# Kernel optimization log

Measured on AMD Instinct MI355X. Metric: run time of the kernel, lower is better.

Reference implementation:

```python
import jax, jax.numpy as jnp
import numpy as np

TEMP = 2.0   # NTXent uses a hardcoded temperature of 2, not the ctor's 0.07
EPS = 1e-8   # F.cosine_similarity eps


def setup_inputs() -> dict:
    key = jax.random.key(0)
    k1, _ = jax.random.split(key)
    x = jax.random.normal(k1, (8192, 256), dtype=jnp.float32)
    unused = jnp.zeros((1,), dtype=jnp.int32)
    return {"x": x, "unused": unused}


def _cos_matrix(a, b):
    # pairwise cosine similarity: [N, N]
    na = jnp.linalg.norm(a, axis=-1)
    nb = jnp.linalg.norm(b, axis=-1)
    dots = a @ b.T
    return dots / jnp.maximum(na[:, None] * nb[None, :], EPS)


def reference(x, unused):
    n = x.shape[0] // 2
    p, q = x[:n], x[n:]  # anchor, positive

    s_pp = _cos_matrix(p, p)
    s_pn = _cos_matrix(p, q)
    s_nn = _cos_matrix(q, q)
    s_np = _cos_matrix(q, p)

    # double loop i, j in [i, n): upper triangle including diagonal
    mask = jnp.triu(jnp.ones((n, n), dtype=bool))

    exp_sum = (jnp.exp(s_pp / TEMP) + jnp.exp(s_pn / TEMP)
               + jnp.exp(s_nn / TEMP) + jnp.exp(s_np / TEMP))
    sim_all = jnp.sum(jnp.where(mask, exp_sum, 0.0))

    sim_s = jnp.sum(jnp.exp(jnp.diagonal(s_pn) / TEMP))

    return -jnp.log(sim_s / sim_all)
```

## Files before the change

### kernel.cpp

```cpp
#include <hip/hip_runtime.h>

#define DIM     256
#define NROWS   8192
#define NTILE   64
#define NBLK    ((NTILE * (NTILE + 1)) / 2)
#define CHPLANE ((size_t)NROWS * 16)

using i32x4  = __attribute__((ext_vector_type(4))) int;
using i32x8  = __attribute__((ext_vector_type(8))) int;
using f32x16 = __attribute__((ext_vector_type(16))) float;

struct i32x8_pair { i32x4 lo, hi; };

__device__ __forceinline__ unsigned fp4q(float v) {
  float a = fabsf(v);
  unsigned s = (__builtin_bit_cast(unsigned, v) >> 31) << 3;
  unsigned c = a < 0.25f ? 0u : a < 0.75f ? 1u : a < 1.25f ? 2u : a < 1.75f ? 3u
             : a < 2.50f ? 4u : a < 3.50f ? 5u : a < 5.00f ? 6u : 7u;
  return s | c;
}

__device__ __forceinline__ void tile_rc(int t, int& bi, int& bj) {
  int i = (int)((129.0 - sqrt(129.0 * 129.0 - 8.0 * (double)t)) * 0.5);
  while ((i * (129 - i)) / 2 > t) --i;
  while (((i + 1) * (128 - i)) / 2 <= t) ++i;
  bi = i;
  bj = i + (t - (i * (129 - i)) / 2);
}

__device__ __forceinline__ float exp_half(float x) {
  float t = x * 0.7213475204444817f;
  float r;
  asm("v_exp_f32 %0, %1" : "=v"(r) : "v"(t));
  return r;
}

__global__ __launch_bounds__(256) void normalize_k(const float* __restrict__ x,
                                                   unsigned char* __restrict__ z4) {
  const int row  = blockIdx.x * 4 + (threadIdx.x >> 6);
  const int lane = threadIdx.x & 63;
  float4 v = ((const float4*)(x + (size_t)row * DIM))[lane];
  float ss = v.x * v.x + v.y * v.y + v.z * v.z + v.w * v.w;
#pragma unroll
  for (int off = 32; off > 0; off >>= 1) ss += __shfl_xor(ss, off, 64);
  float rn = rsqrtf(fmaxf(ss, 1e-24f)) * 16.0f;
  unsigned c0 = fp4q(v.x * rn), c1 = fp4q(v.y * rn);
  unsigned c2 = fp4q(v.z * rn), c3 = fp4q(v.w * rn);
  unsigned short pk = (unsigned short)((c0 | (c1 << 4)) | ((c2 | (c3 << 4)) << 8));
  *(unsigned short*)(z4 + (size_t)(lane >> 3) * CHPLANE
                        + (size_t)row * 16 + ((2 * lane) & 14)) = pk;
}

__global__ __launch_bounds__(256, 3) void gram_k(const unsigned char* __restrict__ z4,
                                                 double2* __restrict__ partial) {
  __shared__ float red[8];

  const int tid   = threadIdx.x;
  const int lane  = tid & 63;
  const int w     = tid >> 6;
  const int wr    = w >> 1, wc = w & 1;
  const int l31   = lane & 31;
  const int khalf = lane >> 5;

  int bi, bj; tile_rc(blockIdx.x, bi, bj);

  const unsigned char* baseA = z4 + (size_t)khalf * CHPLANE
                             + ((size_t)bi * 128 + wr * 64 + l31) * 16;
  const unsigned char* baseB = z4 + (size_t)khalf * CHPLANE
                             + ((size_t)bj * 128 + wc * 64 + l31) * 16;

  f32x16 acc_f[2][2] = {};
  const i32x4 zero4 = {0, 0, 0, 0};
#pragma unroll
  for (int kc = 0; kc < 4; ++kc) {
    i32x8 a[2], b[2];
#pragma unroll
    for (int t = 0; t < 2; ++t) {
      i32x8_pair pa = { *(const i32x4*)(baseA + (size_t)(2 * kc) * CHPLANE + t * 32 * 16),
                        zero4 };
      a[t] = __builtin_bit_cast(i32x8, pa);
      i32x8_pair pb = { *(const i32x4*)(baseB + (size_t)(2 * kc) * CHPLANE + t * 32 * 16),
                        zero4 };
      b[t] = __builtin_bit_cast(i32x8, pb);
    }
#pragma unroll
    for (int ti = 0; ti < 2; ++ti)
#pragma unroll
      for (int tj = 0; tj < 2; ++tj)
        acc_f[ti][tj] = __builtin_amdgcn_mfma_scale_f32_32x32x64_f8f6f4(
            a[ti], b[tj], acc_f[ti][tj],
            4, 4,
            0, 0x7B7B7B7B,
            0, 0x7B7B7B7B);
  }

  const bool tdiag = (bi == bj);
  const bool sdiag = (bj == bi + 32);
  float lsum = 0.0f, dsum = 0.0f;
  if (tdiag || sdiag) {
#pragma unroll
    for (int ti = 0; ti < 2; ++ti)
#pragma unroll
      for (int tj = 0; tj < 2; ++tj)
#pragma unroll
        for (int r = 0; r < 16; ++r) {
          float e = exp_half(acc_f[ti][tj][r]);
          lsum += e;
          int row_l = (r & 3) + 8 * (r >> 2) + 4 * khalf;
          if (wr == wc && ti == tj && row_l == l31) dsum += e;
        }
  } else {
#pragma unroll
    for (int ti = 0; ti < 2; ++ti)
#pragma unroll
      for (int tj = 0; tj < 2; ++tj)
#pragma unroll
        for (int r = 0; r < 16; ++r)
          lsum += exp_half(acc_f[ti][tj][r]);
  }
#pragma unroll
  for (int off = 32; off > 0; off >>= 1) lsum += __shfl_xor(lsum, off, 64);
  if (tdiag || sdiag) {
#pragma unroll
    for (int off = 32; off > 0; off >>= 1) dsum += __shfl_xor(dsum, off, 64);
  }
  if (lane == 0) { red[w] = lsum; red[4 + w] = dsum; }
  __syncthreads();

  if (tid == 0) {
    float l  = red[0] + red[1] + red[2] + red[3];
    float dd = red[4] + red[5] + red[6] + red[7];
    double2 v;
    v.x = tdiag ? (double)l + (double)dd : 2.0 * (double)l;
    v.y = sdiag ? (double)dd : 0.0;
    partial[blockIdx.x] = v;
  }
}

__global__ __launch_bounds__(256) void reduce_k(const double2* __restrict__ partial,
                                               float* __restrict__ out) {
  __shared__ double redS[4], redD[4];
  double s = 0.0, ss = 0.0;
  for (int i = threadIdx.x; i < NBLK; i += 256) {
    double2 v = partial[i];
    s += v.x; ss += v.y;
  }
#pragma unroll
  for (int off = 32; off > 0; off >>= 1) {
    s  += __shfl_xor(s,  off, 64);
    ss += __shfl_xor(ss, off, 64);
  }
  const int w = threadIdx.x >> 6;
  if ((threadIdx.x & 63) == 0) { redS[w] = s; redD[w] = ss; }
  __syncthreads();
  if (threadIdx.x == 0) {
    double S  = redS[0] + redS[1] + redS[2] + redS[3];
    double sd = redD[0] + redD[1] + redD[2] + redD[3];
    out[0] = (float)(log(0.5 * S + sd) - log(sd));
  }
}

extern "C" void kernel_launch(void* const* d_in, const int* in_sizes, int n_in,
                              void* d_out, int out_size, void* d_ws, size_t ws_size,
                              hipStream_t stream) {
  const float* x    = (const float*)d_in[0];
  unsigned char* z4 = (unsigned char*)d_ws;
  double2* partial  = (double2*)((char*)d_ws + 8 * CHPLANE);
  float* out        = (float*)d_out;

  normalize_k<<<dim3(NROWS / 4), dim3(256), 0, stream>>>(x, z4);
  gram_k<<<dim3(NBLK), dim3(256), 0, stream>>>(z4, partial);
  reduce_k<<<dim3(1), dim3(256), 0, stream>>>(partial, out);
}
```

Measured before the change: 74.33 us.

## Process two tiles per gram block, per-wave partials, batch rows in normalize

Each gram block now handles two upper-triangle tiles in sequence and writes one partial per wave, which removes the shared-memory reduction and the __syncthreads. Per-wave sums are kept in double across both tiles, and the exp sums are split over four float accumulators. The normalize kernel now handles 8 rows per wave with 256 blocks instead of 2048, and gram occupancy is raised to 4 blocks per CU. This trades fewer launches and less sync for less parallelism per launch and register pressure from the higher occupancy target.

```diff
diff --git a/kernel.cpp b/kernel.cpp
--- a/kernel.cpp
+++ b/kernel.cpp
@@ -4,6 +4,8 @@
 #define NROWS   8192
 #define NTILE   64
 #define NBLK    ((NTILE * (NTILE + 1)) / 2)
+#define GB      1040
+#define NPART   (GB * 4)
 #define CHPLANE ((size_t)NROWS * 16)
 
 using i32x4  = __attribute__((ext_vector_type(4))) int;
@@ -37,24 +39,27 @@
 
 __global__ __launch_bounds__(256) void normalize_k(const float* __restrict__ x,
                                                    unsigned char* __restrict__ z4) {
-  const int row  = blockIdx.x * 4 + (threadIdx.x >> 6);
+  const int w    = threadIdx.x >> 6;
   const int lane = threadIdx.x & 63;
-  float4 v = ((const float4*)(x + (size_t)row * DIM))[lane];
-  float ss = v.x * v.x + v.y * v.y + v.z * v.z + v.w * v.w;
+  const int row0 = blockIdx.x * 32 + w * 8;
 #pragma unroll
-  for (int off = 32; off > 0; off >>= 1) ss += __shfl_xor(ss, off, 64);
-  float rn = rsqrtf(fmaxf(ss, 1e-24f)) * 16.0f;
-  unsigned c0 = fp4q(v.x * rn), c1 = fp4q(v.y * rn);
-  unsigned c2 = fp4q(v.z * rn), c3 = fp4q(v.w * rn);
-  unsigned short pk = (unsigned short)((c0 | (c1 << 4)) | ((c2 | (c3 << 4)) << 8));
-  *(unsigned short*)(z4 + (size_t)(lane >> 3) * CHPLANE
-                        + (size_t)row * 16 + ((2 * lane) & 14)) = pk;
+  for (int r = 0; r < 8; ++r) {
+    const int row = row0 + r;
+    float4 v = ((const float4*)(x + (size_t)row * DIM))[lane];
+    float ss = v.x * v.x + v.y * v.y + v.z * v.z + v.w * v.w;
+#pragma unroll
+    for (int off = 32; off > 0; off >>= 1) ss += __shfl_xor(ss, off, 64);
+    float rn = rsqrtf(fmaxf(ss, 1e-24f)) * 16.0f;
+    unsigned c0 = fp4q(v.x * rn), c1 = fp4q(v.y * rn);
+    unsigned c2 = fp4q(v.z * rn), c3 = fp4q(v.w * rn);
+    unsigned short pk = (unsigned short)((c0 | (c1 << 4)) | ((c2 | (c3 << 4)) << 8));
+    *(unsigned short*)(z4 + (size_t)(lane >> 3) * CHPLANE
+                          + (size_t)row * 16 + ((2 * lane) & 14)) = pk;
+  }
 }
 
-__global__ __launch_bounds__(256, 3) void gram_k(const unsigned char* __restrict__ z4,
+__global__ __launch_bounds__(256, 4) void gram_k(const unsigned char* __restrict__ z4,
                                                  double2* __restrict__ partial) {
-  __shared__ float red[8];
-
   const int tid   = threadIdx.x;
   const int lane  = tid & 63;
   const int w     = tid >> 6;
@@ -62,78 +67,79 @@
   const int l31   = lane & 31;
   const int khalf = lane >> 5;
 
-  int bi, bj; tile_rc(blockIdx.x, bi, bj);
+  double accS = 0.0, accD = 0.0;
+  const i32x4 zero4 = {0, 0, 0, 0};
 
-  const unsigned char* baseA = z4 + (size_t)khalf * CHPLANE
-                             + ((size_t)bi * 128 + wr * 64 + l31) * 16;
-  const unsigned char* baseB = z4 + (size_t)khalf * CHPLANE
-                             + ((size_t)bj * 128 + wc * 64 + l31) * 16;
+  for (int k = 0; k < 2; ++k) {
+    int bi, bj; tile_rc(blockIdx.x * 2 + k, bi, bj);
 
-  f32x16 acc_f[2][2] = {};
-  const i32x4 zero4 = {0, 0, 0, 0};
+    const unsigned char* baseA = z4 + (size_t)khalf * CHPLANE
+                               + ((size_t)bi * 128 + wr * 64 + l31) * 16;
+    const unsigned char* baseB = z4 + (size_t)khalf * CHPLANE
+                               + ((size_t)bj * 128 + wc * 64 + l31) * 16;
+
+    f32x16 acc_f[2][2] = {};
 #pragma unroll
-  for (int kc = 0; kc < 4; ++kc) {
-    i32x8 a[2], b[2];
+    for (int kc = 0; kc < 4; ++kc) {
+      i32x8 a[2], b[2];
 #pragma unroll
-    for (int t = 0; t < 2; ++t) {
-      i32x8_pair pa = { *(const i32x4*)(baseA + (size_t)(2 * kc) * CHPLANE + t * 32 * 16),
-                        zero4 };
-      a[t] = __builtin_bit_cast(i32x8, pa);
-      i32x8_pair pb = { *(const i32x4*)(baseB + (size_t)(2 * kc) * CHPLANE + t * 32 * 16),
-                        zero4 };
-      b[t] = __builtin_bit_cast(i32x8, pb);
+      for (int t = 0; t < 2; ++t) {
+        i32x8_pair pa = { *(const i32x4*)(baseA + (size_t)(2 * kc) * CHPLANE + t * 512),
+                          zero4 };
+        a[t] = __builtin_bit_cast(i32x8, pa);
+        i32x8_pair pb = { *(const i32x4*)(baseB + (size_t)(2 * kc) * CHPLANE + t * 512),
+                          zero4 };
+        b[t] = __builtin_bit_cast(i32x8, pb);
+      }
+#pragma unroll
+      for (int ti = 0; ti < 2; ++ti)
+#pragma unroll
+        for (int tj = 0; tj < 2; ++tj)
+          acc_f[ti][tj] = __builtin_amdgcn_mfma_scale_f32_32x32x64_f8f6f4(
+              a[ti], b[tj], acc_f[ti][tj],
+              4, 4,
+              0, 0x7B7B7B7B,
+              0, 0x7B7B7B7B);
     }
+
+    const bool tdiag = (bi == bj);
+    const bool sdiag = (bj == bi + 32);
+    float ls[4] = {0.f, 0.f, 0.f, 0.f};
+    float dsum = 0.0f;
+    if (tdiag || sdiag) {
 #pragma unroll
-    for (int ti = 0; ti < 2; ++ti)
+      for (int ti = 0; ti < 2; ++ti)
 #pragma unroll
-      for (int tj = 0; tj < 2; ++tj)
-        acc_f[ti][tj] = __builtin_amdgcn_mfma_scale_f32_32x32x64_f8f6f4(
-            a[ti], b[tj], acc_f[ti][tj],
-            4, 4,
-            0, 0x7B7B7B7B,
-            0, 0x7B7B7B7B);
+        for (int tj = 0; tj < 2; ++tj)
+#pragma unroll
+          for (int r = 0; r < 16; ++r) {
+            float e = exp_half(acc_f[ti][tj][r]);
+            ls[r & 3] += e;
+            int row_l = (r & 3) + 8 * (r >> 2) + 4 * khalf;
+            if (wr == wc && ti == tj && row_l == l31) dsum += e;
+          }
+    } else {
+#pragma unroll
+      for (int ti = 0; ti < 2; ++ti)
+#pragma unroll
+        for (int tj = 0; tj < 2; ++tj)
+#pragma unroll
+          for (int r = 0; r < 16; ++r)
+            ls[r & 3] += exp_half(acc_f[ti][tj][r]);
+    }
+    float lsum = (ls[0] + ls[1]) + (ls[2] + ls[3]);
+    accS += tdiag ? (double)lsum + (double)dsum : 2.0 * (double)lsum;
+    if (sdiag) accD += (double)dsum;
   }
 
-  const bool tdiag = (bi == bj);
-  const bool sdiag = (bj == bi + 32);
-  float lsum = 0.0f, dsum = 0.0f;
-  if (tdiag || sdiag) {
 #pragma unroll
-    for (int ti = 0; ti < 2; ++ti)
-#pragma unroll
-      for (int tj = 0; tj < 2; ++tj)
-#pragma unroll
-        for (int r = 0; r < 16; ++r) {
-          float e = exp_half(acc_f[ti][tj][r]);
-          lsum += e;
-          int row_l = (r & 3) + 8 * (r >> 2) + 4 * khalf;
-          if (wr == wc && ti == tj && row_l == l31) dsum += e;
-        }
-  } else {
-#pragma unroll
-    for (int ti = 0; ti < 2; ++ti)
-#pragma unroll
-      for (int tj = 0; tj < 2; ++tj)
-#pragma unroll
-        for (int r = 0; r < 16; ++r)
-          lsum += exp_half(acc_f[ti][tj][r]);
+  for (int off = 32; off > 0; off >>= 1) {
+    accS += __shfl_xor(accS, off, 64);
+    accD += __shfl_xor(accD, off, 64);
   }
-#pragma unroll
-  for (int off = 32; off > 0; off >>= 1) lsum += __shfl_xor(lsum, off, 64);
-  if (tdiag || sdiag) {
-#pragma unroll
-    for (int off = 32; off > 0; off >>= 1) dsum += __shfl_xor(dsum, off, 64);
-  }
-  if (lane == 0) { red[w] = lsum; red[4 + w] = dsum; }
-  __syncthreads();
-
-  if (tid == 0) {
-    float l  = red[0] + red[1] + red[2] + red[3];
-    float dd = red[4] + red[5] + red[6] + red[7];
-    double2 v;
-    v.x = tdiag ? (double)l + (double)dd : 2.0 * (double)l;
-    v.y = sdiag ? (double)dd : 0.0;
-    partial[blockIdx.x] = v;
+  if (lane == 0) {
+    double2 v; v.x = accS; v.y = accD;
+    partial[blockIdx.x * 4 + w] = v;
   }
 }
 
@@ -141,7 +147,7 @@
                                                float* __restrict__ out) {
   __shared__ double redS[4], redD[4];
   double s = 0.0, ss = 0.0;
-  for (int i = threadIdx.x; i < NBLK; i += 256) {
+  for (int i = threadIdx.x; i < NPART; i += 256) {
     double2 v = partial[i];
     s += v.x; ss += v.y;
   }
@@ -168,7 +174,7 @@
   double2* partial  = (double2*)((char*)d_ws + 8 * CHPLANE);
   float* out        = (float*)d_out;
 
-  normalize_k<<<dim3(NROWS / 4), dim3(256), 0, stream>>>(x, z4);
-  gram_k<<<dim3(NBLK), dim3(256), 0, stream>>>(z4, partial);
-  reduce_k<<<dim3(1), dim3(256), 0, stream>>>(partial, out);
+  normalize_k<<<dim3(256),  dim3(256), 0, stream>>>(x, z4);
+  gram_k<<<dim3(GB),        dim3(256), 0, stream>>>(z4, partial);
+  reduce_k<<<dim3(1),       dim3(256), 0, stream>>>(partial, out);
 }
```

New measurement: 82.07 us. 10.4% more time.
